# Performance work log

Measured on AMD Instinct MI355X. Metric: run time of the kernel, lower is better.

## Reference

```python
import jax, jax.numpy as jnp
import numpy as np

H = 12      # num_heads
EPS = 1e-5  # LayerNorm eps (torch default)


def _ln(x, g, b):
    m = x.mean(-1, keepdims=True)
    v = x.var(-1, keepdims=True)
    return (x - m) * jax.lax.rsqrt(v + EPS) * g + b


def _rot_half(x):
    x1, x2 = x[..., 0::2], x[..., 1::2]
    return jnp.stack((-x2, x1), axis=-1).reshape(x.shape)


def _rope_tables(n, head_dim):
    # rotary-embedding-torch: RotaryEmbedding(dim=head_dim//2, use_xpos=True),
    # theta=10000, scale_base=512. Only first rot=head_dim//2 dims are rotated.
    rot = head_dim // 2
    inv = 1.0 / (10000.0 ** (jnp.arange(0, rot, 2, dtype=jnp.float32) / rot))
    t = jnp.arange(n, dtype=jnp.float32)
    freqs = jnp.repeat(t[:, None] * inv[None, :], 2, axis=-1)  # (n, rot), interleaved
    base = (jnp.arange(0, rot, 2, dtype=jnp.float32) + 0.4 * rot) / (1.4 * rot)
    power = (t - n // 2) / 512.0
    sc = base[None, :] ** power[:, None]
    sc = jnp.concatenate([sc, sc], axis=-1)  # (n, rot), concatenated (library behavior)
    return jnp.cos(freqs), jnp.sin(freqs), sc


def _attn_path(xn, Wqkv, bqkv, Wproj, bproj, qg, qb, kg, kb, R, rg, rb):
    B, N, D = xn.shape
    d = D // H
    qkv = xn @ Wqkv + bqkv
    q, k, v = jnp.split(qkv, 3, axis=-1)
    hd = lambda t: t.reshape(B, N, H, d).transpose(0, 2, 1, 3)  # (B,H,N,d)
    q, k, v = hd(q), hd(k), hd(v)
    q = _ln(q, qg, qb)  # per-head QK LayerNorm
    k = _ln(k, kg, kb)
    cos, sin, sc = _rope_tables(N, d)
    rot = d // 2

    def rope(t, s):  # rotate only first rot dims
        tl, tr = t[..., :rot], t[..., rot:]
        tl = tl * cos * s + _rot_half(tl) * sin * s
        return jnp.concatenate([tl, tr], axis=-1)

    q = rope(q, sc)
    v = rope(v, 1.0 / sc)  # source applies rope to (q, v), not k

    scores = jnp.einsum('bhid,bhjd->bhij', q, k) / jnp.sqrt(jnp.asarray(d, xn.dtype))
    p = jax.nn.softmax(scores, axis=-1)
    # SDPA(q,k,ones_NN)[...,i,j] == sum_k p[...,i,k] for every j (constant over j).
    # All downstream ops (head-mix einsum, LayerNorm over heads, @ v) therefore
    # reduce exactly to the per-(b,i) computation below, avoiding an N^3 matmul.
    s = p.sum(-1)                              # (B,H,N)
    mix = jnp.einsum('bhi,hg->big', s, R)      # (B,N,H)
    w = _ln(mix, rg, rb)                       # reattn LayerNorm over head axis
    vsum = v.sum(axis=2)                       # (B,H,d); (w @ v) with w const over j
    y = jnp.einsum('big,bgd->bigd', w, vsum).reshape(B, N, D)
    return y @ Wproj + bproj


def _cgmlp(xn, W1, b1, gg, gb, cw, cb, W2, b2):
    h = jax.nn.gelu(xn @ W1 + b1, approximate=False)
    c2 = h.shape[-1] // 2
    xr, xg = h[..., :c2], h[..., c2:]
    xg = _ln(xg, gg, gb).transpose(0, 2, 1)  # (B,C,T)
    K = cw.shape[-1]
    xg = jax.lax.conv_general_dilated(xg, cw, (1,), [((K - 1) // 2, (K - 1) // 2)],
                                      dimension_numbers=('NCH', 'OIH', 'NCH'),
                                      feature_group_count=c2)  # depthwise conv1d
    xg = (xg + cb[None, :, None]).transpose(0, 2, 1)
    return (xr * xg) @ W2 + b2


def reference(x, Wqkv, bqkv, Wproj, bproj, qn_g, qn_b, kn_g, kn_b, reattn_w, rn_g, rn_b,
              ln1_g, ln1_b, ln2_g, ln2_b, ls1, ls2, W1, b1, gn_g, gn_b, conv_w, conv_b,
              W2, b2, Wout, bout):
    # eval mode: dropout / drop_path are identity
    xa = _ln(x, ln1_g, ln1_b)
    attn = sum(_attn_path(xa, Wqkv[p], bqkv[p], Wproj[p], bproj[p], qn_g[p], qn_b[p],
                          kn_g[p], kn_b[p], reattn_w[p], rn_g[p], rn_b[p])
               for p in range(2))
    x_attn = x + ls1 * attn
    xm = _ln(x, ln2_g, ln2_b)
    x_mlp = x + ls2 * _cgmlp(xm, W1, b1, gn_g, gn_b, conv_w, conv_b, W2, b2)
    xf = jnp.concatenate([x_attn, x_mlp], axis=-1)
    return xf @ Wout + bout + x


def setup_inputs():
    B, N, D, P = 4, 1024, 768, 2
    d = D // H
    C = 4 * D
    c2 = C // 2
    K = 21
    ks = iter(jax.random.split(jax.random.key(0), 16))
    nrm = lambda s, sd=0.02: jax.random.normal(next(ks), s, jnp.float32) * sd
    return {
        'x': jax.random.normal(next(ks), (B, N, D), jnp.float32),
        'Wqkv': nrm((P, D, 3 * D)), 'bqkv': jnp.zeros((P, 3 * D)),
        'Wproj': nrm((P, D, D)), 'bproj': jnp.zeros((P, D)),
        'qn_g': jnp.ones((P, d)), 'qn_b': jnp.zeros((P, d)),
        'kn_g': jnp.ones((P, d)), 'kn_b': jnp.zeros((P, d)),
        'reattn_w': jax.random.normal(next(ks), (P, H, H), jnp.float32),
        'rn_g': jnp.ones((P, H)), 'rn_b': jnp.zeros((P, H)),
        'ln1_g': jnp.ones((D,)), 'ln1_b': jnp.zeros((D,)),
        'ln2_g': jnp.ones((D,)), 'ln2_b': jnp.zeros((D,)),
        'ls1': jnp.full((D,), 0.01, jnp.float32), 'ls2': jnp.full((D,), 0.01, jnp.float32),
        'W1': nrm((D, C)), 'b1': jnp.zeros((C,)),
        'gn_g': jnp.ones((c2,)), 'gn_b': jnp.zeros((c2,)),
        'conv_w': nrm((c2, 1, K), 0.1), 'conv_b': jnp.zeros((c2,)),
        'W2': nrm((c2, D)), 'b2': jnp.zeros((D,)),
        'Wout': nrm((2 * D, D)), 'bout': jnp.zeros((D,)),
    }
```

## Files before the change

### kernel.cpp

```cpp
#include <hip/hip_runtime.h>
#include <hip/hip_bf16.h>

typedef short s16x8 __attribute__((ext_vector_type(8)));
typedef float f32x4 __attribute__((ext_vector_type(4)));

#define C2 1536

__device__ __forceinline__ float b2f(ushort u){ return __uint_as_float(((unsigned)u)<<16); }
__device__ __forceinline__ ushort f2b(float f){ unsigned u = __float_as_uint(f); return (ushort)((u + 0x7fffu + ((u>>16)&1u)) >> 16); }

#define GL16(g, l) __builtin_amdgcn_global_load_lds( \
    (const __attribute__((address_space(1))) void*)(g), \
    (__attribute__((address_space(3))) void*)(l), 16, 0, 0)

#define VMW(n) asm volatile("s_waitcnt vmcnt(" #n ")" ::: "memory")
#define LGW()  asm volatile("s_waitcnt lgkmcnt(0)" ::: "memory")
#define SB()   __builtin_amdgcn_sched_barrier(0)
#define BAR()  __builtin_amdgcn_s_barrier()
#define SP1    __builtin_amdgcn_s_setprio(1)
#define SP0    __builtin_amdgcn_s_setprio(0)
#define MF(va, vb, c) __builtin_amdgcn_mfma_f32_16x16x32_bf16(va, vb, c, 0,0,0)

#define RDA(P, mh) { const int ab = (P) + aro + (mh)*4096; \
    a0=L8(ab+sx0);      a1=L8(ab+sx1); \
    a2=L8(ab+1024+sx0); a3=L8(ab+1024+sx1); \
    a4=L8(ab+2048+sx0); a5=L8(ab+2048+sx1); \
    a6=L8(ab+3072+sx0); a7=L8(ab+3072+sx1); }
#define RDB0(P, nh) { const int bb = (P) + bro + (nh)*2048; \
    b00=L8(bb+sx0); b01=L8(bb+sx1); b02=L8(bb+1024+sx0); b03=L8(bb+1024+sx1); }
#define RDB1(P, nh) { const int bb = (P) + bro + (nh)*2048; \
    b10=L8(bb+sx0); b11=L8(bb+sx1); b12=L8(bb+1024+sx0); b13=L8(bb+1024+sx1); }
#define L8(off) (*(const s16x8*)&lds[off])
#define STG(p0, p1, T, dstb) { \
    GL16((p0) + (size_t)(T)*64, &lds[(dstb) + ldsw]); \
    GL16((p1) + (size_t)(T)*64, &lds[(dstb) + 4096 + ldsw]); }
#define QD(mh, nh, B0,B1,B2,B3) { \
  acc[(mh)*4+0][(nh)*2+0]=MF(a0,B0,acc[(mh)*4+0][(nh)*2+0]); \
  acc[(mh)*4+0][(nh)*2+0]=MF(a1,B1,acc[(mh)*4+0][(nh)*2+0]); \
  acc[(mh)*4+0][(nh)*2+1]=MF(a0,B2,acc[(mh)*4+0][(nh)*2+1]); \
  acc[(mh)*4+0][(nh)*2+1]=MF(a1,B3,acc[(mh)*4+0][(nh)*2+1]); \
  acc[(mh)*4+1][(nh)*2+0]=MF(a2,B0,acc[(mh)*4+1][(nh)*2+0]); \
  acc[(mh)*4+1][(nh)*2+0]=MF(a3,B1,acc[(mh)*4+1][(nh)*2+0]); \
  acc[(mh)*4+1][(nh)*2+1]=MF(a2,B2,acc[(mh)*4+1][(nh)*2+1]); \
  acc[(mh)*4+1][(nh)*2+1]=MF(a3,B3,acc[(mh)*4+1][(nh)*2+1]); \
  acc[(mh)*4+2][(nh)*2+0]=MF(a4,B0,acc[(mh)*4+2][(nh)*2+0]); \
  acc[(mh)*4+2][(nh)*2+0]=MF(a5,B1,acc[(mh)*4+2][(nh)*2+0]); \
  acc[(mh)*4+2][(nh)*2+1]=MF(a4,B2,acc[(mh)*4+2][(nh)*2+1]); \
  acc[(mh)*4+2][(nh)*2+1]=MF(a5,B3,acc[(mh)*4+2][(nh)*2+1]); \
  acc[(mh)*4+3][(nh)*2+0]=MF(a6,B0,acc[(mh)*4+3][(nh)*2+0]); \
  acc[(mh)*4+3][(nh)*2+0]=MF(a7,B1,acc[(mh)*4+3][(nh)*2+0]); \
  acc[(mh)*4+3][(nh)*2+1]=MF(a6,B2,acc[(mh)*4+3][(nh)*2+1]); \
  acc[(mh)*4+3][(nh)*2+1]=MF(a7,B3,acc[(mh)*4+3][(nh)*2+1]); }

#define EIGHT(t0, t1, DS, VM4) \
   VMW(4); BAR(); \
  RDA(0,0); RDB0(0,0); \
  STG(pA00,pA01,(t1), 16384); \
  LGW(); SB(); SP1; QD(0,0,b00,b01,b02,b03); SP0; BAR(); \
   RDB1(0,1); \
  STG(pA10,pA11,(t1), 24576); \
  BAR(); LGW(); SB(); SP1; QD(0,1,b10,b11,b12,b13); SP0; BAR(); \
   RDA(0,1); \
  if (DS) { STG(pB00,pB01,(t0)+2, 32768); } \
  BAR(); LGW(); SB(); SP1; QD(1,0,b00,b01,b02,b03); SP0; BAR(); \
   if (DS) { STG(pB10,pB11,(t0)+2, 40960); } \
  BAR(); SP1; QD(1,1,b10,b11,b12,b13); SP0; BAR(); \
   VM4; BAR(); \
  RDA(16384,0); RDB0(16384,0); \
  if (DS) { STG(pA00,pA01,(t0)+2, 0); } \
  LGW(); SB(); SP1; QD(0,0,b00,b01,b02,b03); SP0; BAR(); \
   RDB1(16384,1); \
  if (DS) { STG(pA10,pA11,(t0)+2, 8192); } \
  BAR(); LGW(); SB(); SP1; QD(0,1,b10,b11,b12,b13); SP0; BAR(); \
   RDA(16384,1); \
  if (DS) { STG(pB00,pB01,(t1)+2, 49152); } \
  BAR(); LGW(); SB(); SP1; QD(1,0,b00,b01,b02,b03); SP0; BAR(); \
   if (DS) { STG(pB10,pB11,(t1)+2, 57344); } \
  BAR(); SP1; QD(1,1,b10,b11,b12,b13); SP0; BAR();

template<int EPI>
__global__ __launch_bounds__(512, 1) void gemm256(
    const ushort* __restrict__ A, const ushort* __restrict__ BT,
    int M, int N, int K,
    const float* __restrict__ bias,
    ushort* __restrict__ o16, ushort* __restrict__ o16b)
{
    extern __shared__ ushort lds[];
    const int t = threadIdx.x;
    const int lane = t & 63, wv = t >> 6;
    const int wr = wv >> 2, wc = wv & 3;
    const int r0 = lane & 15, q = lane >> 4, e7 = lane & 7;
    const int m0 = blockIdx.y*256, n0 = blockIdx.x*256;

    const int idx = wv*64 + lane;
    const int lr8 = idx >> 3;
    const int ksrc = (idx & 7) ^ (lr8 & 7);
    const ushort* pA00 = A  + (size_t)(m0 +   0 +  0 + lr8)*K + ksrc*8;
    const ushort* pA01 = A  + (size_t)(m0 +   0 + 64 + lr8)*K + ksrc*8;
    const ushort* pA10 = A  + (size_t)(m0 + 128 +  0 + lr8)*K + ksrc*8;
    const ushort* pA11 = A  + (size_t)(m0 + 128 + 64 + lr8)*K + ksrc*8;
    const ushort* pB00 = BT + (size_t)(n0 +   0 +  0 + lr8)*K + ksrc*8;
    const ushort* pB01 = BT + (size_t)(n0 +   0 + 64 + lr8)*K + ksrc*8;
    const ushort* pB10 = BT + (size_t)(n0 + 128 +  0 + lr8)*K + ksrc*8;
    const ushort* pB11 = BT + (size_t)(n0 + 128 + 64 + lr8)*K + ksrc*8;
    const int ldsw = wv*512;

    const int aro = (wr*128 + r0)*64;
    const int bro = 32768 + (wc*64 + r0)*64;
    const int sx0 = (q ^ e7)*8, sx1 = ((q ^ e7)*8) ^ 32;

    f32x4 acc[8][4];
    #pragma unroll
    for (int i=0;i<8;++i)
        #pragma unroll
        for (int j=0;j<4;++j) acc[i][j] = (f32x4){0.f,0.f,0.f,0.f};
    s16x8 a0,a1,a2,a3,a4,a5,a6,a7;
    s16x8 b00,b01,b02,b03, b10,b11,b12,b13;

    const int nkt = K >> 6;
    const int niter = nkt >> 1;

    STG(pB00,pB01, 0, 32768);
    STG(pB10,pB11, 0, 40960);
    STG(pA00,pA01, 0, 0);
    STG(pA10,pA11, 0, 8192);
    STG(pB00,pB01, 1, 49152);
    STG(pB10,pB11, 1, 57344);

    for (int i = 0; i < niter-1; ++i) {
        const int t0 = 2*i, t1 = 2*i+1;
        EIGHT(t0, t1, 1, VMW(4));
    }
    {
        const int t0 = nkt-2, t1 = nkt-1;
        EIGHT(t0, t1, 0, VMW(0));
    }

    #pragma unroll
    for (int gm=0; gm<8; ++gm) {
        #pragma unroll
        for (int gn=0; gn<4; ++gn) {
            int col = n0 + wc*64 + gn*16 + r0;
            #pragma unroll
            for (int r=0; r<4; ++r) {
                int row = m0 + wr*128 + gm*16 + q*4 + r;
                float v = acc[gm][gn][r];
                if (EPI == 0) {
                    o16[(size_t)row*N + col] = f2b(v + bias[col]);
                } else {
                    v += bias[col];
                    float g = 0.5f*v*(1.0f + erff(v*0.70710678118f));
                    if (col < C2) o16 [(size_t)row*C2 + col]        = f2b(g);
                    else          o16b[(size_t)row*C2 + (col - C2)] = f2b(g);
                }
            }
        }
    }
}

template<int EPI>
__global__ __launch_bounds__(256) void gemm_bf16(
    const ushort* __restrict__ A, const ushort* __restrict__ BT,
    int M, int N, int K,
    const float* __restrict__ bias, const float* __restrict__ scale,
    const float* __restrict__ xres,
    ushort* __restrict__ o16, float* __restrict__ o32)
{
    __shared__ ushort Al[2][128*32];
    __shared__ ushort Bl[2][128*32];
    const int t = threadIdx.x;
    const int m0 = blockIdx.y*128, n0 = blockIdx.x*128;
    const int lane = t & 63, wv = t >> 6;
    const int wm = (wv>>1)*64, wn = (wv&1)*64;
    const int r0 = lane & 15, q = lane >> 4;

    const int c0i = t, c1i = t + 256;
    const int lrow0 = ((c0i>>6)<<4) | (c0i&15), lkc0 = ((c0i>>4)&3) << 3;
    const int lrow1 = ((c1i>>6)<<4) | (c1i&15), lkc1 = ((c1i>>4)&3) << 3;
    const ushort* gA0 = A  + (size_t)(m0+lrow0)*K + lkc0;
    const ushort* gB0 = BT + (size_t)(n0+lrow0)*K + lkc0;
    const ushort* gA1 = A  + (size_t)(m0+lrow1)*K + lkc1;
    const ushort* gB1 = BT + (size_t)(n0+lrow1)*K + lkc1;

    f32x4 acc[4][4];
    #pragma unroll
    for (int i=0;i<4;++i)
        #pragma unroll
        for (int j=0;j<4;++j) acc[i][j] = (f32x4){0.f,0.f,0.f,0.f};

    const int nkt = K >> 5;
    uint4 pa0_0, pb0_0, pa1_0, pb1_0;
    uint4 pa0_1, pb0_1, pa1_1, pb1_1;
    pa0_0 = *(const uint4*)gA0;        pb0_0 = *(const uint4*)gB0;
    pa1_0 = *(const uint4*)gA1;        pb1_0 = *(const uint4*)gB1;
    pa0_1 = *(const uint4*)(gA0 + 32); pb0_1 = *(const uint4*)(gB0 + 32);
    pa1_1 = *(const uint4*)(gA1 + 32); pb1_1 = *(const uint4*)(gB1 + 32);
    *(uint4*)&Al[0][c0i*8] = pa0_0;
    *(uint4*)&Bl[0][c0i*8] = pb0_0;
    *(uint4*)&Al[0][c1i*8] = pa1_0;
    *(uint4*)&Bl[0][c1i*8] = pb1_0;

    for (int kt = 0; kt < nkt; kt += 2) {
        __syncthreads();
        {
            s16x8 af[4], bfr[4];
            #pragma unroll
            for (int mt=0; mt<4; ++mt) af[mt]  = *(const s16x8*)&Al[0][(((wm>>4)+mt)*64 + lane)*8];
            #pragma unroll
            for (int nt=0; nt<4; ++nt) bfr[nt] = *(const s16x8*)&Bl[0][(((wn>>4)+nt)*64 + lane)*8];
            *(uint4*)&Al[1][c0i*8] = pa0_1;
            *(uint4*)&Bl[1][c0i*8] = pb0_1;
            *(uint4*)&Al[1][c1i*8] = pa1_1;
            *(uint4*)&Bl[1][c1i*8] = pb1_1;
            if (kt+2 < nkt) {
                pa0_0 = *(const uint4*)(gA0 + (kt+2)*32);
                pb0_0 = *(const uint4*)(gB0 + (kt+2)*32);
                pa1_0 = *(const uint4*)(gA1 + (kt+2)*32);
                pb1_0 = *(const uint4*)(gB1 + (kt+2)*32);
            }
            #pragma unroll
            for (int mt=0; mt<4; ++mt)
                #pragma unroll
                for (int nt=0; nt<4; ++nt)
                    acc[mt][nt] = __builtin_amdgcn_mfma_f32_16x16x32_bf16(af[mt], bfr[nt], acc[mt][nt], 0,0,0);
        }
        __syncthreads();
        {
            s16x8 af[4], bfr[4];
            #pragma unroll
            for (int mt=0; mt<4; ++mt) af[mt]  = *(const s16x8*)&Al[1][(((wm>>4)+mt)*64 + lane)*8];
            #pragma unroll
            for (int nt=0; nt<4; ++nt) bfr[nt] = *(const s16x8*)&Bl[1][(((wn>>4)+nt)*64 + lane)*8];
            if (kt+2 < nkt) {
                *(uint4*)&Al[0][c0i*8] = pa0_0;
                *(uint4*)&Bl[0][c0i*8] = pb0_0;
                *(uint4*)&Al[0][c1i*8] = pa1_0;
                *(uint4*)&Bl[0][c1i*8] = pb1_0;
            }
            if (kt+3 < nkt) {
                pa0_1 = *(const uint4*)(gA0 + (kt+3)*32);
                pb0_1 = *(const uint4*)(gB0 + (kt+3)*32);
                pa1_1 = *(const uint4*)(gA1 + (kt+3)*32);
                pb1_1 = *(const uint4*)(gB1 + (kt+3)*32);
            }
            #pragma unroll
            for (int mt=0; mt<4; ++mt)
                #pragma unroll
                for (int nt=0; nt<4; ++nt)
                    acc[mt][nt] = __builtin_amdgcn_mfma_f32_16x16x32_bf16(af[mt], bfr[nt], acc[mt][nt], 0,0,0);
        }
    }

    #pragma unroll
    for (int mt=0; mt<4; ++mt) {
        #pragma unroll
        for (int nt=0; nt<4; ++nt) {
            int col = n0 + wn + nt*16 + r0;
            #pragma unroll
            for (int r=0; r<4; ++r) {
                int row = m0 + wm + mt*16 + q*4 + r;
                float v = acc[mt][nt][r];
                if (EPI == 2) {
                    v += bias[col];
                    o16[(size_t)row*1536 + 768 + col] = f2b(xres[(size_t)row*768 + col] + scale[col]*v);
                } else {
                    o32[(size_t)row*768 + col] = v + bias[col] + xres[(size_t)row*768 + col];
                }
            }
        }
    }
}

__global__ __launch_bounds__(256) void pack_bt(const float* __restrict__ src, ushort* __restrict__ dst,
                                               int K, int ld, int coff)
{
    __shared__ float tl[32*33];
    int kt = blockIdx.x*32, nt = blockIdx.y*32;
    int nl = threadIdx.x & 31, kg = threadIdx.x >> 5;
    #pragma unroll
    for (int kk=0; kk<4; ++kk) {
        int k = kg*4 + kk;
        tl[k*33 + nl] = src[(size_t)(kt + k)*ld + coff + nt + nl];
    }
    __syncthreads();
    int kcol = threadIdx.x & 31, ng = threadIdx.x >> 5;
    #pragma unroll
    for (int nn=0; nn<4; ++nn) {
        int nrow = ng*4 + nn;
        dst[(size_t)(nt + nrow)*K + kt + kcol] = f2b(tl[kcol*33 + nrow]);
    }
}

__global__ __launch_bounds__(256) void pack_bv(const float* __restrict__ bqkv, float* __restrict__ bvp)
{
    int idx = blockIdx.x*256 + threadIdx.x;
    if (idx < 1536) bvp[idx] = bqkv[(idx/768)*2304 + 1536 + (idx%768)];
}

__global__ __launch_bounds__(256) void ln_x_kernel(const float* __restrict__ x,
    const float* __restrict__ g1, const float* __restrict__ b1,
    const float* __restrict__ g2, const float* __restrict__ b2,
    ushort* __restrict__ xa, ushort* __restrict__ xm)
{
    __shared__ float sb[8];
    int row = blockIdx.x; int t = threadIdx.x;
    float v[3]; float s = 0.f, ss = 0.f;
    #pragma unroll
    for (int e=0; e<3; ++e) { v[e] = x[(size_t)row*768 + t + e*256]; s += v[e]; ss += v[e]*v[e]; }
    for (int o=32; o>0; o>>=1){ s += __shfl_down(s,o,64); ss += __shfl_down(ss,o,64); }
    int lane = t&63, w = t>>6;
    if (lane==0){ sb[w]=s; sb[4+w]=ss; }
    __syncthreads();
    s = sb[0]+sb[1]+sb[2]+sb[3]; ss = sb[4]+sb[5]+sb[6]+sb[7];
    float mean = s*(1.f/768.f);
    float var  = ss*(1.f/768.f) - mean*mean;
    float rstd = rsqrtf(var + 1e-5f);
    #pragma unroll
    for (int e=0; e<3; ++e){
        int c = t + e*256;
        float n = (v[e]-mean)*rstd;
        xa[(size_t)row*768 + c] = f2b(n*g1[c] + b1[c]);
        xm[(size_t)row*768 + c] = f2b(n*g2[c] + b2[c]);
    }
}

__global__ __launch_bounds__(256) void prep_kernel(
    float* __restrict__ w1t, float* __restrict__ w2t, float* __restrict__ wvec,
    float* __restrict__ attn_c, float* __restrict__ vsum,
    const float* __restrict__ R, const float* __restrict__ rng,
    const float* __restrict__ rnb, const float* __restrict__ bproj)
{
    int idx = blockIdx.x*256 + threadIdx.x;
    {
        int i = idx >> 6, j = idx & 63;
        float w1, w2;
        if (j < 32) {
            int m = j >> 1;
            float inv = powf(10000.f, -(float)m*(1.f/16.f));
            float fr = (float)i * inv;
            float c = cosf(fr), sn = sinf(fr);
            float power = ((float)i - 512.f) * (1.f/512.f);
            float basev = (2.f*(float)(j & 15) + 12.8f) * (1.f/44.8f);
            float sfac = powf(basev, -power);
            w1 = c * sfac;
            w2 = ((j & 1) ? sn : -sn) * sfac;
        } else { w1 = 1.f; w2 = 0.f; }
        w1t[idx] = w1; w2t[idx] = w2;
    }
    if (blockIdx.x >= 1 && blockIdx.x <= 12) {
        int k = (blockIdx.x-1)*256 + threadIdx.x;
        int o = k % 768;
        attn_c[k] = bproj[o] + bproj[768 + o];
    }
    if (blockIdx.x >= 13 && blockIdx.x <= 36) {
        int k = (blockIdx.x-13)*256 + threadIdx.x;
        vsum[k] = 0.f;
    }
    if (blockIdx.x == 0) {
        __shared__ float mixs[24];
        __shared__ float ws[24];
        int t = threadIdx.x;
        if (t < 24) {
            int p = t / 12, g = t % 12;
            float m = 0.f;
            for (int h=0; h<12; ++h) m += R[p*144 + h*12 + g];
            mixs[t] = m;
        }
        __syncthreads();
        if (t < 2) {
            float mean=0.f, var=0.f;
            for (int g=0; g<12; ++g) mean += mixs[t*12+g];
            mean *= (1.f/12.f);
            for (int g=0; g<12; ++g){ float d = mixs[t*12+g]-mean; var += d*d; }
            var *= (1.f/12.f);
            float rstd = rsqrtf(var + 1e-5f);
            for (int g=0; g<12; ++g)
                ws[t*12+g] = (mixs[t*12+g]-mean)*rstd*rng[t*12+g] + rnb[t*12+g];
        }
        __syncthreads();
        if (t < 24) wvec[t] = ws[t];
    }
}

__global__ __launch_bounds__(256) void rope_reduce(const ushort* __restrict__ V,
    const float* __restrict__ w1t, const float* __restrict__ w2t, float* __restrict__ vsum)
{
    int col = blockIdx.x*256 + threadIdx.x;
    int b = blockIdx.y;
    int i0 = blockIdx.z * 256;
    int j = col & 63;
    float acc = 0.f;
    const ushort* vp = V + (size_t)(b*1024 + i0)*1536;
    #pragma unroll 4
    for (int i=0; i<256; ++i) {
        float v1 = b2f(vp[(size_t)i*1536 + col]);
        float v2 = b2f(vp[(size_t)i*1536 + (col^1)]);
        int ii = i0 + i;
        acc += w1t[ii*64 + j]*v1 + w2t[ii*64 + j]*v2;
    }
    atomicAdd(&vsum[b*1536 + col], acc);
}

__global__ __launch_bounds__(256) void attn_gemm(const float* __restrict__ vsum,
    const float* __restrict__ wvec, const float* __restrict__ Wproj, float* __restrict__ attn_c)
{
    int o  = blockIdx.x*256 + threadIdx.x;
    int c0 = blockIdx.y * 96;
    int b  = blockIdx.z;
    int p  = c0 / 768;
    float acc = 0.f;
    #pragma unroll 4
    for (int cc=0; cc<96; ++cc) {
        int c = c0 + cc;
        int cl = c - p*768;
        float y = wvec[p*12 + (cl>>6)] * vsum[b*1536 + c];
        acc += y * Wproj[(size_t)p*589824 + (size_t)cl*768 + o];
    }
    atomicAdd(&attn_c[b*768 + o], acc);
}

__global__ __launch_bounds__(256) void xf_left(const float* __restrict__ x, const float* __restrict__ ls1,
    const float* __restrict__ attn_c, ushort* __restrict__ xf)
{
    int col = blockIdx.x*256 + threadIdx.x;
    int row = blockIdx.y;
    xf[(size_t)row*1536 + col] = f2b(x[(size_t)row*768 + col] + ls1[col]*attn_c[(row>>10)*768 + col]);
}

__global__ __launch_bounds__(256) void ln_gate(const ushort* __restrict__ xg,
    const float* __restrict__ g, const float* __restrict__ bta, ushort* __restrict__ out)
{
    __shared__ float sb[8];
    int row = blockIdx.x, t = threadIdx.x;
    float v[6]; float s=0.f, ss=0.f;
    #pragma unroll
    for (int e=0;e<6;++e){ v[e] = b2f(xg[(size_t)row*1536 + t + e*256]); s+=v[e]; ss+=v[e]*v[e]; }
    for (int o=32; o>0; o>>=1){ s += __shfl_down(s,o,64); ss += __shfl_down(ss,o,64); }
    int lane = t&63, w = t>>6;
    if (lane==0){ sb[w]=s; sb[4+w]=ss; }
    __syncthreads();
    s = sb[0]+sb[1]+sb[2]+sb[3]; ss = sb[4]+sb[5]+sb[6]+sb[7];
    float mean = s*(1.f/1536.f);
    float var  = ss*(1.f/1536.f) - mean*mean;
    float rstd = rsqrtf(var + 1e-5f);
    #pragma unroll
    for (int e=0;e<6;++e){
        int c = t + e*256;
        out[(size_t)row*1536 + c] = f2b((v[e]-mean)*rstd*g[c] + bta[c]);
    }
}

#define CROWS 128
#define CIN   (CROWS + 20)
#define CSTR  72
__global__ __launch_bounds__(256) void conv_mul(const ushort* __restrict__ xgln,
    const float* __restrict__ cw, const float* __restrict__ cb,
    const ushort* __restrict__ xr, ushort* __restrict__ u)
{
    __shared__ ushort tile[CIN * CSTR];
    const int c0 = blockIdx.x * 64;
    const int i0 = blockIdx.y * CROWS;
    const int b  = blockIdx.z;
    const int t  = threadIdx.x;
    const size_t base = (size_t)b*1024*1536;

    #pragma unroll
    for (int it = 0; it < 5; ++it) {
        int idx = it*256 + t;
        if (idx < CIN*8) {
            int r  = idx >> 3;
            int cq = (idx & 7) * 8;
            int si = i0 + r - 10;
            uint4 val = make_uint4(0u,0u,0u,0u);
            if (si >= 0 && si < 1024)
                val = *(const uint4*)(xgln + base + (size_t)si*1536 + c0 + cq);
            *(uint4*)&tile[r*CSTR + cq] = val;
        }
    }
    __syncthreads();

    const int ch = t & 63;
    const int o0 = (t >> 6) * 32;
    const int c  = c0 + ch;

    float w[21];
    #pragma unroll
    for (int k=0; k<21; ++k) w[k] = cw[c*21 + k];
    const float bias = cb[c];

    float win[21];
    #pragma unroll
    for (int j=0; j<20; ++j) win[j] = b2f(tile[(o0+j)*CSTR + ch]);

    #pragma unroll
    for (int j=0; j<32; ++j) {
        win[(j+20)%21] = b2f(tile[(o0+j+20)*CSTR + ch]);
        float acc = bias;
        #pragma unroll
        for (int k=0; k<21; ++k) acc += win[(j+k)%21] * w[k];
        size_t off = base + (size_t)(i0+o0+j)*1536 + c;
        u[off] = f2b(b2f(xr[off]) * acc);
    }
}

extern "C" void kernel_launch(void* const* d_in, const int* in_sizes, int n_in,
                              void* d_out, int out_size, void* d_ws, size_t ws_size,
                              hipStream_t stream)
{
    const float* x     = (const float*)d_in[0];
    const float* Wqkv  = (const float*)d_in[1];
    const float* bqkv  = (const float*)d_in[2];
    const float* Wproj = (const float*)d_in[3];
    const float* bproj = (const float*)d_in[4];
    const float* Rw    = (const float*)d_in[9];
    const float* rng   = (const float*)d_in[10];
    const float* rnb   = (const float*)d_in[11];
    const float* ln1g  = (const float*)d_in[12];
    const float* ln1b  = (const float*)d_in[13];
    const float* ln2g  = (const float*)d_in[14];
    const float* ln2b  = (const float*)d_in[15];
    const float* ls1   = (const float*)d_in[16];
    const float* ls2   = (const float*)d_in[17];
    const float* W1    = (const float*)d_in[18];
    const float* b1    = (const float*)d_in[19];
    const float* gng   = (const float*)d_in[20];
    const float* gnb   = (const float*)d_in[21];
    const float* cw    = (const float*)d_in[22];
    const float* cb    = (const float*)d_in[23];
    const float* W2    = (const float*)d_in[24];
    const float* b2    = (const float*)d_in[25];
    const float* Wout  = (const float*)d_in[26];
    const float* bout  = (const float*)d_in[27];
    float* out = (float*)d_out;

    char* ws = (char*)d_ws;
    size_t off = 0;
    auto alloc = [&](size_t bytes)->char* {
        char* p = ws + off;
        off += (bytes + 255) & ~(size_t)255;
        return p;
    };
    ushort* WvT   = (ushort*)alloc(1536*768*2);
    ushort* W1T   = (ushort*)alloc(3072*768*2);
    ushort* W2T   = (ushort*)alloc(768*1536*2);
    ushort* WoutT = (ushort*)alloc(768*1536*2);
    float*  bvp   = (float*)alloc(1536*4);
    float*  w1t   = (float*)alloc(65536*4);
    float*  w2t   = (float*)alloc(65536*4);
    float*  wvec  = (float*)alloc(24*4);
    float*  attnc = (float*)alloc(3072*4);
    float*  vsum  = (float*)alloc(6144*4);
    ushort* xa16  = (ushort*)alloc(4096*768*2);
    ushort* xm16  = (ushort*)alloc(4096*768*2);
    ushort* V16   = (ushort*)alloc(4096*1536*2);
    ushort* xg16  = (ushort*)alloc(4096*1536*2);
    ushort* xf16  = (ushort*)alloc(4096*1536*2);
    ushort* xgln  = xa16;
    ushort* xr16  = V16;
    ushort* u16   = xg16;
    (void)ws_size; (void)n_in; (void)in_sizes; (void)out_size;

    (void)hipFuncSetAttribute((const void*)gemm256<0>, hipFuncAttributeMaxDynamicSharedMemorySize, 131072);
    (void)hipFuncSetAttribute((const void*)gemm256<1>, hipFuncAttributeMaxDynamicSharedMemorySize, 131072);

    for (int p = 0; p < 2; ++p)
        pack_bt<<<dim3(24, 24), 256, 0, stream>>>(Wqkv + (size_t)p*768*2304, WvT + (size_t)p*768*768,
                                                  768, 2304, 1536);
    pack_bt<<<dim3(24, 96), 256, 0, stream>>>(W1,   W1T,   768,  3072, 0);
    pack_bt<<<dim3(48, 24), 256, 0, stream>>>(W2,   W2T,   1536, 768,  0);
    pack_bt<<<dim3(48, 24), 256, 0, stream>>>(Wout, WoutT, 1536, 768,  0);
    pack_bv<<<dim3(6), 256, 0, stream>>>(bqkv, bvp);
    prep_kernel<<<dim3(256), 256, 0, stream>>>(w1t, w2t, wvec, attnc, vsum, Rw, rng, rnb, bproj);

    ln_x_kernel<<<dim3(4096), 256, 0, stream>>>(x, ln1g, ln1b, ln2g, ln2b, xa16, xm16);

    gemm256<0><<<dim3(6, 16), 512, 131072, stream>>>(xa16, WvT, 4096, 1536, 768,
                                                     bvp, V16, nullptr);
    rope_reduce<<<dim3(6, 4, 4), 256, 0, stream>>>(V16, w1t, w2t, vsum);
    attn_gemm<<<dim3(3, 16, 4), 256, 0, stream>>>(vsum, wvec, Wproj, attnc);
    xf_left<<<dim3(3, 4096), 256, 0, stream>>>(x, ls1, attnc, xf16);

    gemm256<1><<<dim3(12, 16), 512, 131072, stream>>>(xm16, W1T, 4096, 3072, 768,
                                                      b1, xr16, xg16);
    ln_gate<<<dim3(4096), 256, 0, stream>>>(xg16, gng, gnb, xgln);
    conv_mul<<<dim3(24, 8, 4), 256, 0, stream>>>(xgln, cw, cb, xr16, u16);
    gemm_bf16<2><<<dim3(6, 32), 256, 0, stream>>>(u16, W2T, 4096, 768, 1536,
                                                  b2, ls2, x, xf16, nullptr);
    gemm_bf16<3><<<dim3(6, 32), 256, 0, stream>>>(xf16, WoutT, 4096, 768, 1536,
                                                  bout, nullptr, x, nullptr, out);
}
```

Measured before the change: 367.7 us.

## Fold W2 and Wout into one combined GEMM over concatenated activations

Previously the block ran W2 (u @ W2 with layer-scale and residual) into a bf16 buffer, then a second GEMM with Wout over the concatenated [xf, xr] buffer. The linear pieces are now folded algebraically: a precomputed (ls2*Wout_bottom)^T @ W2^T weight, summed Wout halves applied to x, and a per-batch constant vector carrying biases and the attention term. This leaves a single K=2304 GEMM over [x, u]. It removes one full activation GEMM and an elementwise pass, but adds per-call weight-folding kernels (including an unoptimized cvec loop) and extra bf16 rounding of the folded weights.

```diff
diff --git a/kernel.cpp b/kernel.cpp
--- a/kernel.cpp
+++ b/kernel.cpp
@@ -161,9 +161,8 @@
 template<int EPI>
 __global__ __launch_bounds__(256) void gemm_bf16(
     const ushort* __restrict__ A, const ushort* __restrict__ BT,
-    int M, int N, int K,
-    const float* __restrict__ bias, const float* __restrict__ scale,
-    const float* __restrict__ xres,
+    int M, int N, int K, int lda, int ldbt,
+    const float* __restrict__ bias, const float* __restrict__ xres,
     ushort* __restrict__ o16, float* __restrict__ o32)
 {
     __shared__ ushort Al[2][128*32];
@@ -177,10 +176,10 @@
     const int c0i = t, c1i = t + 256;
     const int lrow0 = ((c0i>>6)<<4) | (c0i&15), lkc0 = ((c0i>>4)&3) << 3;
     const int lrow1 = ((c1i>>6)<<4) | (c1i&15), lkc1 = ((c1i>>4)&3) << 3;
-    const ushort* gA0 = A  + (size_t)(m0+lrow0)*K + lkc0;
-    const ushort* gB0 = BT + (size_t)(n0+lrow0)*K + lkc0;
-    const ushort* gA1 = A  + (size_t)(m0+lrow1)*K + lkc1;
-    const ushort* gB1 = BT + (size_t)(n0+lrow1)*K + lkc1;
+    const ushort* gA0 = A  + (size_t)(m0+lrow0)*lda + lkc0;
+    const ushort* gB0 = BT + (size_t)(n0+lrow0)*ldbt + lkc0;
+    const ushort* gA1 = A  + (size_t)(m0+lrow1)*lda + lkc1;
+    const ushort* gB1 = BT + (size_t)(n0+lrow1)*ldbt + lkc1;
 
     f32x4 acc[4][4];
     #pragma unroll
@@ -260,11 +259,10 @@
             for (int r=0; r<4; ++r) {
                 int row = m0 + wm + mt*16 + q*4 + r;
                 float v = acc[mt][nt][r];
-                if (EPI == 2) {
-                    v += bias[col];
-                    o16[(size_t)row*1536 + 768 + col] = f2b(xres[(size_t)row*768 + col] + scale[col]*v);
+                if (EPI == 3) {
+                    o32[(size_t)row*768 + col] = v + bias[(row>>10)*768 + col] + xres[(size_t)row*768 + col];
                 } else {
-                    o32[(size_t)row*768 + col] = v + bias[col] + xres[(size_t)row*768 + col];
+                    o16[(size_t)row*2304 + 768 + col] = f2b(v);
                 }
             }
         }
@@ -291,16 +289,76 @@
     }
 }
 
+__global__ __launch_bounds__(256) void pack_bts(const float* __restrict__ src,
+    const float* __restrict__ scale, ushort* __restrict__ dst)
+{
+    __shared__ float tl[32*33];
+    int kt = blockIdx.x*32, nt = blockIdx.y*32;
+    int nl = threadIdx.x & 31, kg = threadIdx.x >> 5;
+    #pragma unroll
+    for (int kk=0; kk<4; ++kk) {
+        int k = kg*4 + kk;
+        tl[k*33 + nl] = src[(size_t)(kt + k)*768 + nt + nl];
+    }
+    __syncthreads();
+    int kcol = threadIdx.x & 31, ng = threadIdx.x >> 5;
+    #pragma unroll
+    for (int nn=0; nn<4; ++nn) {
+        int nrow = ng*4 + nn;
+        dst[(size_t)(nt + nrow)*768 + kt + kcol] = f2b(tl[kcol*33 + nrow] * scale[kt + kcol]);
+    }
+}
+
+__global__ __launch_bounds__(256) void fold1_pack(const float* __restrict__ Wout, ushort* __restrict__ dst)
+{
+    __shared__ float tl[32*33];
+    int kt = blockIdx.x*32, nt = blockIdx.y*32;
+    int nl = threadIdx.x & 31, kg = threadIdx.x >> 5;
+    #pragma unroll
+    for (int kk=0; kk<4; ++kk) {
+        int k = kg*4 + kk;
+        tl[k*33 + nl] = Wout[(size_t)(kt + k)*768 + nt + nl]
+                      + Wout[(size_t)(768 + kt + k)*768 + nt + nl];
+    }
+    __syncthreads();
+    int kcol = threadIdx.x & 31, ng = threadIdx.x >> 5;
+    #pragma unroll
+    for (int nn=0; nn<4; ++nn) {
+        int nrow = ng*4 + nn;
+        dst[(size_t)(nt + nrow)*2304 + kt + kcol] = f2b(tl[kcol*33 + nrow]);
+    }
+}
+
+__global__ __launch_bounds__(256) void cast16(const float* __restrict__ src, ushort* __restrict__ dst, int n)
+{
+    int i = blockIdx.x*256 + threadIdx.x;
+    if (i < n) dst[i] = f2b(src[i]);
+}
+
 __global__ __launch_bounds__(256) void pack_bv(const float* __restrict__ bqkv, float* __restrict__ bvp)
 {
     int idx = blockIdx.x*256 + threadIdx.x;
     if (idx < 1536) bvp[idx] = bqkv[(idx/768)*2304 + 1536 + (idx%768)];
+}
+
+__global__ __launch_bounds__(256) void cvec_kernel(const float* __restrict__ attn_c,
+    const float* __restrict__ ls1, const float* __restrict__ ls2, const float* __restrict__ b2,
+    const float* __restrict__ bout, const float* __restrict__ Wout, float* __restrict__ cvecb)
+{
+    int o = blockIdx.x*256 + threadIdx.x;
+    int b = blockIdx.y;
+    float acc = bout[o];
+    for (int d = 0; d < 768; ++d) {
+        acc += ls2[d]*b2[d]*Wout[(size_t)(768+d)*768 + o];
+        acc += ls1[d]*attn_c[b*768 + d]*Wout[(size_t)d*768 + o];
+    }
+    cvecb[b*768 + o] = acc;
 }
 
 __global__ __launch_bounds__(256) void ln_x_kernel(const float* __restrict__ x,
     const float* __restrict__ g1, const float* __restrict__ b1,
     const float* __restrict__ g2, const float* __restrict__ b2,
-    ushort* __restrict__ xa, ushort* __restrict__ xm)
+    ushort* __restrict__ xa, ushort* __restrict__ xm, ushort* __restrict__ xc)
 {
     __shared__ float sb[8];
     int row = blockIdx.x; int t = threadIdx.x;
@@ -321,6 +379,7 @@
         float n = (v[e]-mean)*rstd;
         xa[(size_t)row*768 + c] = f2b(n*g1[c] + b1[c]);
         xm[(size_t)row*768 + c] = f2b(n*g2[c] + b2[c]);
+        xc[(size_t)row*2304 + c] = f2b(v[e]);
     }
 }
 
@@ -419,14 +478,6 @@
     atomicAdd(&attn_c[b*768 + o], acc);
 }
 
-__global__ __launch_bounds__(256) void xf_left(const float* __restrict__ x, const float* __restrict__ ls1,
-    const float* __restrict__ attn_c, ushort* __restrict__ xf)
-{
-    int col = blockIdx.x*256 + threadIdx.x;
-    int row = blockIdx.y;
-    xf[(size_t)row*1536 + col] = f2b(x[(size_t)row*768 + col] + ls1[col]*attn_c[(row>>10)*768 + col]);
-}
-
 __global__ __launch_bounds__(256) void ln_gate(const ushort* __restrict__ xg,
     const float* __restrict__ g, const float* __restrict__ bta, ushort* __restrict__ out)
 {
@@ -498,8 +549,8 @@
         float acc = bias;
         #pragma unroll
         for (int k=0; k<21; ++k) acc += win[(j+k)%21] * w[k];
-        size_t off = base + (size_t)(i0+o0+j)*1536 + c;
-        u[off] = f2b(b2f(xr[off]) * acc);
+        size_t offr = base + (size_t)(i0+o0+j)*1536 + c;
+        u[(size_t)(b*1024 + i0+o0+j)*2304 + 768 + c] = f2b(b2f(xr[offr]) * acc);
     }
 }
 
@@ -542,22 +593,23 @@
     };
     ushort* WvT   = (ushort*)alloc(1536*768*2);
     ushort* W1T   = (ushort*)alloc(3072*768*2);
-    ushort* W2T   = (ushort*)alloc(768*1536*2);
-    ushort* WoutT = (ushort*)alloc(768*1536*2);
+    ushort* BT2   = (ushort*)alloc(1536*768*2);
+    ushort* Afold = (ushort*)alloc(768*768*2);
+    ushort* BTf   = (ushort*)alloc(768*2304*2);
     float*  bvp   = (float*)alloc(1536*4);
     float*  w1t   = (float*)alloc(65536*4);
     float*  w2t   = (float*)alloc(65536*4);
     float*  wvec  = (float*)alloc(24*4);
     float*  attnc = (float*)alloc(3072*4);
     float*  vsum  = (float*)alloc(6144*4);
+    float*  cvecb = (float*)alloc(3072*4);
     ushort* xa16  = (ushort*)alloc(4096*768*2);
     ushort* xm16  = (ushort*)alloc(4096*768*2);
     ushort* V16   = (ushort*)alloc(4096*1536*2);
     ushort* xg16  = (ushort*)alloc(4096*1536*2);
-    ushort* xf16  = (ushort*)alloc(4096*1536*2);
+    ushort* xcat  = (ushort*)alloc((size_t)4096*2304*2);
     ushort* xgln  = xa16;
     ushort* xr16  = V16;
-    ushort* u16   = xg16;
     (void)ws_size; (void)n_in; (void)in_sizes; (void)out_size;
 
     (void)hipFuncSetAttribute((const void*)gemm256<0>, hipFuncAttributeMaxDynamicSharedMemorySize, 131072);
@@ -566,26 +618,29 @@
     for (int p = 0; p < 2; ++p)
         pack_bt<<<dim3(24, 24), 256, 0, stream>>>(Wqkv + (size_t)p*768*2304, WvT + (size_t)p*768*768,
                                                   768, 2304, 1536);
-    pack_bt<<<dim3(24, 96), 256, 0, stream>>>(W1,   W1T,   768,  3072, 0);
-    pack_bt<<<dim3(48, 24), 256, 0, stream>>>(W2,   W2T,   1536, 768,  0);
-    pack_bt<<<dim3(48, 24), 256, 0, stream>>>(Wout, WoutT, 1536, 768,  0);
+    pack_bt<<<dim3(24, 96), 256, 0, stream>>>(W1, W1T, 768, 3072, 0);
     pack_bv<<<dim3(6), 256, 0, stream>>>(bqkv, bvp);
     prep_kernel<<<dim3(256), 256, 0, stream>>>(w1t, w2t, wvec, attnc, vsum, Rw, rng, rnb, bproj);
 
-    ln_x_kernel<<<dim3(4096), 256, 0, stream>>>(x, ln1g, ln1b, ln2g, ln2b, xa16, xm16);
+    fold1_pack<<<dim3(24, 24), 256, 0, stream>>>(Wout, BTf);
+    pack_bts<<<dim3(24, 24), 256, 0, stream>>>(Wout + (size_t)768*768, ls2, Afold);
+    cast16<<<dim3(4608), 256, 0, stream>>>(W2, BT2, 1536*768);
+    gemm_bf16<4><<<dim3(12, 6), 256, 0, stream>>>(Afold, BT2, 768, 1536, 768, 768, 768,
+                                                  nullptr, nullptr, BTf, nullptr);
+
+    ln_x_kernel<<<dim3(4096), 256, 0, stream>>>(x, ln1g, ln1b, ln2g, ln2b, xa16, xm16, xcat);
 
     gemm256<0><<<dim3(6, 16), 512, 131072, stream>>>(xa16, WvT, 4096, 1536, 768,
                                                      bvp, V16, nullptr);
     rope_reduce<<<dim3(6, 4, 4), 256, 0, stream>>>(V16, w1t, w2t, vsum);
     attn_gemm<<<dim3(3, 16, 4), 256, 0, stream>>>(vsum, wvec, Wproj, attnc);
-    xf_left<<<dim3(3, 4096), 256, 0, stream>>>(x, ls1, attnc, xf16);
+    cvec_kernel<<<dim3(3, 4), 256, 0, stream>>>(attnc, ls1, ls2, b2, bout, Wout, cvecb);
 
     gemm256<1><<<dim3(12, 16), 512, 131072, stream>>>(xm16, W1T, 4096, 3072, 768,
                                                       b1, xr16, xg16);
     ln_gate<<<dim3(4096), 256, 0, stream>>>(xg16, gng, gnb, xgln);
-    conv_mul<<<dim3(24, 8, 4), 256, 0, stream>>>(xgln, cw, cb, xr16, u16);
-    gemm_bf16<2><<<dim3(6, 32), 256, 0, stream>>>(u16, W2T, 4096, 768, 1536,
-                                                  b2, ls2, x, xf16, nullptr);
-    gemm_bf16<3><<<dim3(6, 32), 256, 0, stream>>>(xf16, WoutT, 4096, 768, 1536,
-                                                  bout, nullptr, x, nullptr, out);
-}
+    conv_mul<<<dim3(24, 8, 4), 256, 0, stream>>>(xgln, cw, cb, xr16, xcat);
+
+    gemm_bf16<3><<<dim3(6, 32), 256, 0, stream>>>(xcat, BTf, 4096, 768, 2304, 2304, 2304,
+                                                  cvecb, x, nullptr, out);
+}
```

After: 431.0 us. 1.17x slower.
